# Performance work log

Hardware: AMD Instinct MI355X
Metric: run time of the kernel (lower is better)

The kernel has to match this reference:

```python
import jax, jax.numpy as jnp
import numpy as np

B, N, D, K = 8, 2048, 512, 16  # batch, points, feature dim, similar_num
EPS = 1e-8


def setup_inputs() -> dict:
    key = jax.random.key(0)
    ks = jax.random.split(key, 9)
    p = jax.random.normal(ks[0], (B, N, 3), dtype=jnp.float32)
    q = jax.random.normal(ks[1], (B, N, 3), dtype=jnp.float32)
    ffp = jax.random.normal(ks[2], (B, N, D), dtype=jnp.float32)
    ffq = jax.random.normal(ks[3], (B, N, D), dtype=jnp.float32)
    eye = jnp.eye(3, dtype=jnp.float32)
    # near-identity perturbed rotations so inverse is well-conditioned
    R1 = eye + 0.1 * jax.random.normal(ks[4], (B, N, 3, 3), dtype=jnp.float32)
    R2 = eye + 0.1 * jax.random.normal(ks[5], (B, N, 3, 3), dtype=jnp.float32)
    centroids = jax.random.randint(ks[6], (B, N), 0, 2 * N)  # FPS indices into 2N pts
    W = 0.02 * jax.random.normal(ks[7], (3, 3 * D), dtype=jnp.float32)  # refine_net pointwise linear
    b = jnp.zeros((3,), dtype=jnp.float32)
    return {"p": p, "q": q, "ffp": ffp, "ffq": ffq, "R1": R1, "R2": R2,
            "centroids": centroids, "W": W, "b": b}


def _forward(p, q, ffp, ffq, R1, R2, centroids, W, b):
    # cosine similarity between query features (ffq) and source features (ffp): [B,N,N]
    fq = ffq / (jnp.linalg.norm(ffq, axis=-1, keepdims=True) + EPS)
    fp = ffp / (jnp.linalg.norm(ffp, axis=-1, keepdims=True) + EPS)
    w1 = jnp.einsum('bqd,bpd->bqp', fq, fp)
    _, idx = jax.lax.top_k(w1, K)                      # [B,N,K] neighbor indices into ffp
    feat = jax.vmap(lambda z, i: z[i])(ffp, idx)       # batched gather -> [B,N,K,D]
    # adaptive_{avg,max}_pool2d over the K axis, then cat(avg, max): [B,N,2D]
    f_agg = jnp.concatenate([feat.mean(axis=2), feat.max(axis=2)], axis=-1)
    f1 = jnp.concatenate([ffq, f_agg], axis=-1)        # [B,N,3D]
    vec = jnp.einsum('bnd,od->bno', f1, W) + b         # refine_net -> [B,N,3]
    vec = jnp.linalg.inv(R1) @ vec[..., None]          # rotate back (R1^-1)
    vec = (jnp.linalg.inv(R2) @ vec)[..., 0]           # rotate back (R2^-1) -> [B,N,3]
    mask = (centroids >= p.shape[1]).astype(vec.dtype)[..., None]
    q_refine = q + vec * mask
    return q_refine, idx


def reference(p, q, ffp, ffq, R1, R2, centroids, W, b):
    q_refine, similar_idx = _forward(p, q, ffp, ffq, R1, R2, centroids, W, b)
    # original returns (q_cat, q_refine, q_refine, similar_idx)
    return (q, q_refine, q_refine, similar_idx)
```

## Files before the change

kernel.cpp:

```cpp
#include <hip/hip_runtime.h>
#include <math.h>

#define BB 8
#define NN 2048
#define DD 512
#define KK 16
#define BN (BB*NN)

#define QT 64
#define JSPLIT 4
#define JRANGE (NN/JSPLIT)
#define MM (16*JSPLIT)
#define SIMP 68

#define KSPLIT 384

#define OUT1 (BN*3)
#define OUT2 (2*BN*3)
#define OUT3 (3*BN*3)

typedef __attribute__((ext_vector_type(8))) short bf16x8;
typedef __attribute__((ext_vector_type(4))) float f32x4;

__device__ inline unsigned short cvt_bf16(float f) {
    unsigned int u = __float_as_uint(f);
    return (unsigned short)((u + 0x7fffu + ((u >> 16) & 1u)) >> 16);
}

__device__ inline void gload_lds16(const unsigned short* g, unsigned short* lds) {
    __builtin_amdgcn_global_load_lds((const __attribute__((address_space(1))) void*)g,
                                     (__attribute__((address_space(3))) void*)lds,
                                     16, 0, 0);
}

__global__ __launch_bounds__(256) void k_norm_np(const float* __restrict__ ffq,
                                                 const float* __restrict__ ffp,
                                                 float* __restrict__ normq,
                                                 float* __restrict__ normp,
                                                 float* __restrict__ rnp32) {
    const int row = blockIdx.x * 32 + (threadIdx.x >> 3);
    const int j   = threadIdx.x & 7;
    const bool isQ = row < BN;
    const int r = isQ ? row : row - BN;
    const float* x = (isQ ? ffq : ffp) + (size_t)r * DD;

    float B[4];
#pragma unroll
    for (int t = 0; t < 4; ++t) {
        const float* xb = x + t * 128;
        float e = xb[j];
        float rj = __fmul_rn(e, e);
#pragma unroll
        for (int i = 1; i < 16; ++i) {
            float v = xb[8 * i + j];
            rj = __fadd_rn(rj, __fmul_rn(v, v));
        }
        float s = __fadd_rn(rj, __shfl_xor(rj, 1, 8));
        float u = __fadd_rn(s,  __shfl_xor(s,  2, 8));
        float w = __fadd_rn(u,  __shfl_xor(u,  4, 8));
        B[t] = w;
    }
    if (j == 0) {
        float norm2 = __fadd_rn(__fadd_rn(B[0], B[1]), __fadd_rn(B[2], B[3]));
        float nrm = __fsqrt_rn(norm2);
        if (isQ) { normq[r] = nrm; }
        else {
            normp[r] = nrm;
            rnp32[r] = 1.0f / __fadd_rn(nrm, 1e-8f);
        }
    }
}

__global__ __launch_bounds__(256) void k_normalize(const float* __restrict__ ffq,
                                                   const float* __restrict__ ffp,
                                                   const float* __restrict__ normq,
                                                   const float* __restrict__ normp,
                                                   float* __restrict__ fqn,
                                                   float* __restrict__ fpn,
                                                   unsigned short* __restrict__ fqb,
                                                   unsigned short* __restrict__ fpb) {
    const size_t e4 = ((size_t)blockIdx.x * 256 + threadIdx.x) * 4;
    if (e4 >= (size_t)BN * DD) return;
    const int row = (int)(e4 >> 9);
    {
        float4 v = *(const float4*)(ffq + e4);
        float den = __fadd_rn(normq[row], 1e-8f);
        float4 o;
        o.x = __fdiv_rn(v.x, den); o.y = __fdiv_rn(v.y, den);
        o.z = __fdiv_rn(v.z, den); o.w = __fdiv_rn(v.w, den);
        *(float4*)(fqn + e4) = o;
        ushort4 b; b.x = cvt_bf16(o.x); b.y = cvt_bf16(o.y);
        b.z = cvt_bf16(o.z); b.w = cvt_bf16(o.w);
        *(ushort4*)(fqb + e4) = b;
    }
    {
        float4 v = *(const float4*)(ffp + e4);
        float den = __fadd_rn(normp[row], 1e-8f);
        float4 o;
        o.x = __fdiv_rn(v.x, den); o.y = __fdiv_rn(v.y, den);
        o.z = __fdiv_rn(v.z, den); o.w = __fdiv_rn(v.w, den);
        *(float4*)(fpn + e4) = o;
        ushort4 b; b.x = cvt_bf16(o.x); b.y = cvt_bf16(o.y);
        b.z = cvt_bf16(o.z); b.w = cvt_bf16(o.w);
        *(ushort4*)(fpb + e4) = b;
    }
}

#define CK 128
__global__ __launch_bounds__(256, 4) void k_phase1_m(const unsigned short* __restrict__ fqb,
                                                     const unsigned short* __restrict__ fpb,
                                                     unsigned short* __restrict__ cand) {
    __shared__ __align__(16) float simb[QT * SIMP];
    __shared__ __align__(16) unsigned short Bst[64 * CK];

    const int b  = blockIdx.x & 7;
    const int i0 = ((blockIdx.x >> 3) & 31) * QT;
    const int js = blockIdx.x >> 8;
    const int tid = threadIdx.x;
    const int w = tid >> 6, lane = tid & 63;
    const int n16 = lane & 15, quad = lane >> 4;

    const unsigned short* Aq = fqb + ((size_t)b * NN + i0 + w * 16 + n16) * DD + quad * 8;

    unsigned long long ktop[16];
#pragma unroll
    for (int r = 0; r < 16; ++r) ktop[r] = 0ull;

    const int qq = tid >> 2;
    const int st = tid & 3;
    const size_t bNN = (size_t)b * NN;

    for (int jt = 0; jt < JRANGE / 64; ++jt) {
        const int j0g = js * JRANGE + jt * 64;

        f32x4 acc[4];
#pragma unroll
        for (int ct = 0; ct < 4; ++ct) acc[ct] = (f32x4){0.f, 0.f, 0.f, 0.f};

        for (int kc = 0; kc < 4; ++kc) {
            __syncthreads();
#pragma unroll
            for (int l = 0; l < 4; ++l) {
                const int r  = (w * 4 + l) * 4 + quad;
                const int sb = n16 ^ (r & 15);
                const unsigned short* gsrc =
                    fpb + (bNN + j0g + r) * DD + kc * CK + sb * 8;
                gload_lds16(gsrc, &Bst[(w * 4 + l) * 512]);
            }
            int koff = kc * 128;
            asm volatile("" : "+v"(koff));
            bf16x8 a0 = *(const bf16x8*)(Aq + koff);
            bf16x8 a1 = *(const bf16x8*)(Aq + koff + 32);
            bf16x8 a2 = *(const bf16x8*)(Aq + koff + 64);
            bf16x8 a3 = *(const bf16x8*)(Aq + koff + 96);
            __syncthreads();
#pragma unroll
            for (int k4 = 0; k4 < 4; ++k4) {
                const bf16x8 af = (k4 == 0) ? a0 : (k4 == 1) ? a1 : (k4 == 2) ? a2 : a3;
#pragma unroll
                for (int ct = 0; ct < 4; ++ct) {
                    const int r  = ct * 16 + n16;
                    const int cb = (k4 * 4 + quad) ^ (r & 15);
                    bf16x8 bfr = *(const bf16x8*)&Bst[r * CK + cb * 8];
                    acc[ct] = __builtin_amdgcn_mfma_f32_16x16x32_bf16(
                        af, bfr, acc[ct], 0, 0, 0);
                }
            }
        }

        __syncthreads();
#pragma unroll
        for (int ct = 0; ct < 4; ++ct)
#pragma unroll
            for (int r = 0; r < 4; ++r)
                simb[(w * 16 + quad * 4 + r) * SIMP + ct * 16 + n16] = acc[ct][r];
        __syncthreads();

        unsigned long long nk[16];
#pragma unroll
        for (int t4 = 0; t4 < 4; ++t4) {
            const float4 v4 = *(const float4*)&simb[qq * SIMP + st * 16 + t4 * 4];
            const float vv[4] = {v4.x, v4.y, v4.z, v4.w};
#pragma unroll
            for (int u = 0; u < 4; ++u) {
                const float cvf = __fadd_rn(vv[u], 0.0f);
                const unsigned int ub  = __float_as_uint(cvf);
                const unsigned int ord = ub ^ (((unsigned int)((int)ub >> 31)) | 0x80000000u);
                const unsigned int jg  = (unsigned int)(j0g + st * 16 + t4 * 4 + u);
                nk[t4 * 4 + u] = ((unsigned long long)ord << 32)
                               | (unsigned long long)(~jg);
            }
        }
#pragma unroll
        for (int k = 2; k <= 16; k <<= 1) {
#pragma unroll
            for (int j = k >> 1; j > 0; j >>= 1) {
#pragma unroll
                for (int i = 0; i < 16; ++i) {
                    const int l = i ^ j;
                    if (l > i) {
                        const bool up = ((i & k) == 0);
                        const unsigned long long a = nk[i], bq = nk[l];
                        const bool sw = up ? (a > bq) : (a < bq);
                        nk[i] = sw ? bq : a;
                        nk[l] = sw ? a : bq;
                    }
                }
            }
        }
        unsigned long long mg[16];
#pragma unroll
        for (int i = 0; i < 16; ++i) {
            const unsigned long long a = ktop[i], bq = nk[15 - i];
            mg[i] = (a > bq) ? a : bq;
        }
#pragma unroll
        for (int j = 8; j > 0; j >>= 1) {
#pragma unroll
            for (int i = 0; i < 16; ++i) {
                const int l = i ^ j;
                if (l > i) {
                    const unsigned long long a = mg[i], bq = mg[l];
                    const bool sw = a > bq;
                    mg[i] = sw ? bq : a;
                    mg[l] = sw ? a : bq;
                }
            }
        }
#pragma unroll
        for (int i = 0; i < 16; ++i) ktop[i] = mg[i];
    }

    __syncthreads();
    int p = 15;
    const size_t base = ((size_t)b * NN + i0 + qq) * MM + (size_t)js * 16;
    for (int m = 0; m < 16; ++m) {
        const unsigned long long myk = (p >= 0) ? ktop[p] : 0ull;
        unsigned long long wk = myk;
        unsigned long long ok;
        ok = __shfl_xor(wk, 1, 4); if (ok > wk) wk = ok;
        ok = __shfl_xor(wk, 2, 4); if (ok > wk) wk = ok;
        if (p >= 0 && myk == wk) --p;
        if (st == 0) cand[base + m] = (unsigned short)(~(unsigned int)wk);
    }
}

#define JTILE 64
#define BK 16
#define LDP 68
__global__ __launch_bounds__(256, 4) void k_phase1_v(const float* __restrict__ ffq,
                                                     const float* __restrict__ ffp,
                                                     const float* __restrict__ rnp32,
                                                     unsigned short* __restrict__ cand) {
    __shared__ __align__(16) float As[BK * LDP];
    __shared__ __align__(16) float Bs[BK * LDP];
    __shared__ __align__(16) float simb[QT * SIMP];

    const int b  = blockIdx.x & 7;
    const int i0 = ((blockIdx.x >> 3) & 31) * QT;
    const int js = blockIdx.x >> 8;
    const int tid = threadIdx.x;
    const int tx = tid & 15, ty = tid >> 4;

    const float* Abase = ffq + ((size_t)b * NN + i0) * DD;
    const float* Bbase = ffp + (size_t)b * NN * DD;

    float tv[16]; int tix[16];
#pragma unroll
    for (int r = 0; r < 16; ++r) { tv[r] = -INFINITY; tix[r] = -1; }

    const int lrow = tid >> 2;
    const int lseg = (tid & 3) * 4;
    const int qq = tid >> 2;
    const int st = tid & 3;

    for (int jt = 0; jt < JRANGE / JTILE; ++jt) {
        const int j0 = js * JRANGE + jt * JTILE;
        float acc[4][4];
#pragma unroll
        for (int r = 0; r < 4; ++r)
#pragma unroll
            for (int c = 0; c < 4; ++c) acc[r][c] = 0.0f;

        for (int kt = 0; kt < DD / BK; ++kt) {
            const int k0 = kt * BK;
            __syncthreads();
            float4 av = *(const float4*)(Abase + (size_t)lrow * DD + k0 + lseg);
            float4 bv = *(const float4*)(Bbase + (size_t)(j0 + lrow) * DD + k0 + lseg);
            As[(lseg + 0) * LDP + lrow] = av.x; As[(lseg + 1) * LDP + lrow] = av.y;
            As[(lseg + 2) * LDP + lrow] = av.z; As[(lseg + 3) * LDP + lrow] = av.w;
            Bs[(lseg + 0) * LDP + lrow] = bv.x; Bs[(lseg + 1) * LDP + lrow] = bv.y;
            Bs[(lseg + 2) * LDP + lrow] = bv.z; Bs[(lseg + 3) * LDP + lrow] = bv.w;
            __syncthreads();
#pragma unroll
            for (int kk = 0; kk < BK; ++kk) {
                const float4 a4 = *(const float4*)&As[kk * LDP + ty * 4];
                const float4 b4 = *(const float4*)&Bs[kk * LDP + tx * 4];
                const float ar[4] = {a4.x, a4.y, a4.z, a4.w};
                const float br[4] = {b4.x, b4.y, b4.z, b4.w};
#pragma unroll
                for (int r = 0; r < 4; ++r)
#pragma unroll
                    for (int c = 0; c < 4; ++c)
                        acc[r][c] = fmaf(ar[r], br[c], acc[r][c]);
            }
        }
        float rp[4];
#pragma unroll
        for (int c = 0; c < 4; ++c) rp[c] = rnp32[b * NN + j0 + tx * 4 + c];
#pragma unroll
        for (int r = 0; r < 4; ++r) {
            float4 v4;
            v4.x = acc[r][0] * rp[0]; v4.y = acc[r][1] * rp[1];
            v4.z = acc[r][2] * rp[2]; v4.w = acc[r][3] * rp[3];
            *(float4*)&simb[(ty * 4 + r) * SIMP + tx * 4] = v4;
        }
        __syncthreads();

#pragma unroll
        for (int t = 0; t < 16; ++t) {
            const int jl = st * 16 + t;
            const float v = simb[qq * SIMP + jl];
            const int jg = j0 + jl;
            if (v > tv[0]) {
#pragma unroll
                for (int r = 0; r < 15; ++r) {
                    const bool up = tv[r + 1] < v;
                    const float nv = up ? tv[r + 1] : ((tv[r] < v) ? v : tv[r]);
                    const int   ni = up ? tix[r + 1] : ((tv[r] < v) ? jg : tix[r]);
                    tv[r] = nv; tix[r] = ni;
                }
                if (tv[15] < v) { tv[15] = v; tix[15] = jg; }
            }
        }
        __syncthreads();
    }

    int p = 15;
    const size_t base = ((size_t)b * NN + i0 + qq) * MM + (size_t)js * 16;
    for (int m = 0; m < 16; ++m) {
        float cv = (p >= 0) ? tv[p] : -INFINITY;
        int   ci = (p >= 0) ? tix[p] : -1;
        float ov; int oi;
        ov = __shfl_xor(cv, 1, 4); oi = __shfl_xor(ci, 1, 4);
        if (ov > cv || (ov == cv && (unsigned)oi < (unsigned)ci)) { cv = ov; ci = oi; }
        ov = __shfl_xor(cv, 2, 4); oi = __shfl_xor(ci, 2, 4);
        if (ov > cv || (ov == cv && (unsigned)oi < (unsigned)ci)) { cv = ov; ci = oi; }
        if (p >= 0 && tv[p] == cv && tix[p] == ci) --p;
        if (st == 0) cand[base + m] = (unsigned short)ci;
    }
}

__device__ inline void inv3_apply(const double* a, double x0, double x1, double x2,
                                  double& y0, double& y1, double& y2) {
    double c00 = a[4]*a[8] - a[5]*a[7];
    double c01 = a[2]*a[7] - a[1]*a[8];
    double c02 = a[1]*a[5] - a[2]*a[4];
    double c10 = a[5]*a[6] - a[3]*a[8];
    double c11 = a[0]*a[8] - a[2]*a[6];
    double c12 = a[2]*a[3] - a[0]*a[5];
    double c20 = a[3]*a[7] - a[4]*a[6];
    double c21 = a[1]*a[6] - a[0]*a[7];
    double c22 = a[0]*a[4] - a[1]*a[3];
    double det = a[0]*c00 + a[1]*c10 + a[2]*c20;
    double id = 1.0 / det;
    y0 = (c00*x0 + c01*x1 + c02*x2) * id;
    y1 = (c10*x0 + c11*x1 + c12*x2) * id;
    y2 = (c20*x0 + c21*x1 + c22*x2) * id;
}

#define STG_S 67
template <bool PRE>
__device__ inline void phase2_body(
        const float* __restrict__ qin, const float* __restrict__ ffq,
        const float* __restrict__ ffp, const float* __restrict__ R1,
        const float* __restrict__ R2, const int* __restrict__ cent,
        const float* __restrict__ W, const float* __restrict__ bvec,
        const float* __restrict__ normq, const float* __restrict__ normp,
        const float* __restrict__ fqn, const float* __restrict__ fpn,
        const unsigned short* __restrict__ cand, float* __restrict__ out) {
    static_assert(KSPLIT == 384, "chunk split at c=6 assumes KSPLIT==384");
    static_assert(MM * STG_S >= 2 * DD, "meanf/maxf overlay needs 2*DD floats");
    const int b = blockIdx.x & 7;
    const int i = blockIdx.x >> 3;
    const int tid = threadIdx.x;
    const size_t qi = (size_t)b * NN + i;

    __shared__ float sfqn[DD];
    __shared__ int cj[MM];
    __shared__ float pden_s[MM];
    __shared__ float sv[MM];
    __shared__ int sel[KK];
    __shared__ __align__(16) float stg[MM * STG_S];
    __shared__ float red[3][4];
    float* const meanf = stg;
    float* const maxf  = stg + DD;

    if (PRE) {
        for (int d = tid; d < DD; d += 256)
            sfqn[d] = fqn[qi * DD + d];
    } else {
        const float qden = __fadd_rn(normq[qi], 1e-8f);
        for (int d = tid; d < DD; d += 256)
            sfqn[d] = __fdiv_rn(ffq[qi * DD + d], qden);
    }
    if (tid < MM) {
        int j = (int)cand[qi * MM + tid];
        cj[tid] = j;
        if (!PRE) pden_s[tid] = __fadd_rn(normp[(size_t)b * NN + j], 1e-8f);
    }
    __syncthreads();

    const int srow = tid >> 2;
    const int slan = tid & 3;
    const float* fprow = (PRE ? fpn : ffp) + ((size_t)b * NN + cj[srow]) * DD;
    const float pd = (!PRE) ? pden_s[tid < MM ? tid : 0] : 1.0f;
    float acc1 = 0.0f, acc2 = 0.0f;

    auto stg_write = [&](const float4* P) {
#pragma unroll
        for (int i4 = 0; i4 < 4; ++i4) {
            const int off = srow * STG_S + i4 * 16 + slan * 4;
            stg[off + 0] = P[i4].x; stg[off + 1] = P[i4].y;
            stg[off + 2] = P[i4].z; stg[off + 3] = P[i4].w;
        }
    };
    auto ld_chunk = [&](float4* P, int c) {
#pragma unroll
        for (int i4 = 0; i4 < 4; ++i4)
            P[i4] = *(const float4*)(fprow + c * 64 + i4 * 16 + slan * 4);
    };
    auto chain = [&](int c, float& acc) {
        const int d0 = c * 64;
        const float* s = stg + tid * STG_S;
        if (PRE) {
#pragma unroll
            for (int k = 0; k < 64; ++k)
                acc = fmaf(sfqn[d0 + k], s[k], acc);
        } else {
#pragma unroll
            for (int k = 0; k < 64; ++k)
                acc = fmaf(sfqn[d0 + k], __fdiv_rn(s[k], pd), acc);
        }
    };

    float4 pA[4], pB[4];
    ld_chunk(pA, 0);
#pragma unroll
    for (int ch = 0; ch < 4; ++ch) {
        {
            const int c0 = 2 * ch;
            stg_write(pA);
            ld_chunk(pB, c0 + 1);
            __syncthreads();
            if (tid < MM) chain(c0, (c0 < 6) ? acc1 : acc2);
            __syncthreads();
        }
        {
            const int c1 = 2 * ch + 1;
            stg_write(pB);
            if (ch < 3) ld_chunk(pA, c1 + 1);
            __syncthreads();
            if (tid < MM) chain(c1, (c1 < 6) ? acc1 : acc2);
            __syncthreads();
        }
    }
    if (tid < MM) sv[tid] = __fadd_rn(acc1, acc2);
    __syncthreads();

    if (tid < MM) {
        const float v = sv[tid]; const int jj = cj[tid];
        int rank = 0;
        for (int t = 0; t < MM; ++t) {
            const float vt = sv[t]; const int jo = cj[t];
            rank += (vt > v) || (vt == v && jo < jj);
        }
        if (rank < KK) {
            sel[rank] = jj;
            out[(size_t)OUT3 + qi * KK + rank] = (float)jj;
        }
    }
    __syncthreads();

    for (int d = tid; d < DD; d += 256) {
        float sum = 0.0f, mx = -INFINITY;
#pragma unroll
        for (int k = 0; k < KK; ++k) {
            float v = ffp[((size_t)b * NN + sel[k]) * DD + d];
            sum += v; mx = fmaxf(mx, v);
        }
        meanf[d] = sum * (1.0f / 16.0f);
        maxf[d]  = mx;
    }
    __syncthreads();

    float a0 = 0.f, a1 = 0.f, a2 = 0.f;
    for (int d = tid; d < DD; d += 256) {
        const float x = ffq[qi * DD + d], m = meanf[d], mx = maxf[d];
        a0 = fmaf(W[d],        x, a0); a0 = fmaf(W[512 + d],        m, a0); a0 = fmaf(W[1024 + d],        mx, a0);
        a1 = fmaf(W[1536 + d], x, a1); a1 = fmaf(W[1536 + 512 + d], m, a1); a1 = fmaf(W[1536 + 1024 + d], mx, a1);
        a2 = fmaf(W[3072 + d], x, a2); a2 = fmaf(W[3072 + 512 + d], m, a2); a2 = fmaf(W[3072 + 1024 + d], mx, a2);
    }
#pragma unroll
    for (int off = 32; off > 0; off >>= 1) {
        a0 += __shfl_down(a0, off, 64);
        a1 += __shfl_down(a1, off, 64);
        a2 += __shfl_down(a2, off, 64);
    }
    const int lane = tid & 63, wid = tid >> 6;
    if (lane == 0) { red[0][wid] = a0; red[1][wid] = a1; red[2][wid] = a2; }
    __syncthreads();

    if (tid == 0) {
        double v0 = (double)bvec[0] + red[0][0] + red[0][1] + red[0][2] + red[0][3];
        double v1 = (double)bvec[1] + red[1][0] + red[1][1] + red[1][2] + red[1][3];
        double v2 = (double)bvec[2] + red[2][0] + red[2][1] + red[2][2] + red[2][3];
        double r1[9], r2[9];
#pragma unroll
        for (int t = 0; t < 9; ++t) { r1[t] = R1[qi * 9 + t]; r2[t] = R2[qi * 9 + t]; }
        double u0, u1, u2, w0, w1, w2;
        inv3_apply(r1, v0, v1, v2, u0, u1, u2);
        inv3_apply(r2, u0, u1, u2, w0, w1, w2);
        const float mask = (cent[qi] >= NN) ? 1.0f : 0.0f;
        const float q0 = qin[qi * 3 + 0], q1 = qin[qi * 3 + 1], q2 = qin[qi * 3 + 2];
        out[qi * 3 + 0] = q0; out[qi * 3 + 1] = q1; out[qi * 3 + 2] = q2;
        const float o0 = q0 + (float)w0 * mask;
        const float o1 = q1 + (float)w1 * mask;
        const float o2 = q2 + (float)w2 * mask;
        out[OUT1 + qi * 3 + 0] = o0; out[OUT1 + qi * 3 + 1] = o1; out[OUT1 + qi * 3 + 2] = o2;
        out[OUT2 + qi * 3 + 0] = o0; out[OUT2 + qi * 3 + 1] = o1; out[OUT2 + qi * 3 + 2] = o2;
    }
}

__global__ __launch_bounds__(256, 8) void k_phase2_f(
        const float* qin, const float* ffq, const float* ffp, const float* R1,
        const float* R2, const int* cent, const float* W, const float* bvec,
        const float* fqn, const float* fpn, const unsigned short* cand, float* out) {
    phase2_body<true>(qin, ffq, ffp, R1, R2, cent, W, bvec,
                      nullptr, nullptr, fqn, fpn, cand, out);
}

__global__ __launch_bounds__(256, 8) void k_phase2_v(
        const float* qin, const float* ffq, const float* ffp, const float* R1,
        const float* R2, const int* cent, const float* W, const float* bvec,
        const float* normq, const float* normp, const unsigned short* cand, float* out) {
    phase2_body<false>(qin, ffq, ffp, R1, R2, cent, W, bvec,
                       normq, normp, nullptr, nullptr, cand, out);
}

extern "C" void kernel_launch(void* const* d_in, const int* in_sizes, int n_in,
                              void* d_out, int out_size, void* d_ws, size_t ws_size,
                              hipStream_t stream) {
    (void)in_sizes; (void)n_in; (void)out_size;
    const float* q   = (const float*)d_in[1];
    const float* ffp = (const float*)d_in[2];
    const float* ffq = (const float*)d_in[3];
    const float* R1  = (const float*)d_in[4];
    const float* R2  = (const float*)d_in[5];
    const int*   ct  = (const int*)d_in[6];
    const float* W   = (const float*)d_in[7];
    const float* bb  = (const float*)d_in[8];
    float* out = (float*)d_out;

    float* normq = (float*)d_ws;
    float* normp = normq + BN;
    float* rnp32 = normp + BN;
    unsigned short* cand = (unsigned short*)(rnp32 + BN);
    float* fqn = (float*)(cand + (size_t)BN * MM);
    float* fpn = fqn + (size_t)BN * DD;
    unsigned short* fqb = (unsigned short*)(fpn + (size_t)BN * DD);
    unsigned short* fpb = fqb + (size_t)BN * DD;

    const size_t need = (size_t)BN * (35 * 4 + 2 * DD * 4 + 2 * DD * 2);

    k_norm_np<<<dim3((2 * BN) / 32), dim3(256), 0, stream>>>(ffq, ffp, normq, normp, rnp32);

    if (ws_size >= need) {
        k_normalize<<<dim3((BN * DD) / 1024), dim3(256), 0, stream>>>(
            ffq, ffp, normq, normp, fqn, fpn, fqb, fpb);
        k_phase1_m<<<dim3(BB * (NN / QT) * JSPLIT), dim3(256), 0, stream>>>(fqb, fpb, cand);
        k_phase2_f<<<dim3(BB * NN), dim3(256), 0, stream>>>(q, ffq, ffp, R1, R2, ct, W, bb,
                                                            fqn, fpn, cand, out);
    } else {
        k_phase1_v<<<dim3(BB * (NN / QT) * JSPLIT), dim3(256), 0, stream>>>(ffq, ffp, rnp32, cand);
        k_phase2_v<<<dim3(BB * NN), dim3(256), 0, stream>>>(q, ffq, ffp, R1, R2, ct, W, bb,
                                                            normq, normp, cand, out);
    }
}
```

Baseline: 426.4 us.

## Run phase-2 rescoring with one wavefront per query and register-held candidate rows

Phase-2 blocks drop from 256 threads to a single 64-thread wavefront, where each lane owns one candidate. Each lane loads its own candidate feature row straight into registers (double-buffered float4 chunks) and computes the dot product there, replacing the shared-memory staging and its block barriers. Removing the cross-wave reduction also removes one shared array and one barrier. The trade-offs are much higher register pressure from 32 float4 buffers and uncoalesced per-lane row loads, with fewer threads left for the gather and projection loops.

```diff
diff --git a/kernel.cpp b/kernel.cpp
--- a/kernel.cpp
+++ b/kernel.cpp
@@ -369,7 +369,6 @@
     y2 = (c20*x0 + c21*x1 + c22*x2) * id;
 }
 
-#define STG_S 67
 template <bool PRE>
 __device__ inline void phase2_body(
         const float* __restrict__ qin, const float* __restrict__ ffq,
@@ -380,109 +379,90 @@
         const float* __restrict__ fqn, const float* __restrict__ fpn,
         const unsigned short* __restrict__ cand, float* __restrict__ out) {
     static_assert(KSPLIT == 384, "chunk split at c=6 assumes KSPLIT==384");
-    static_assert(MM * STG_S >= 2 * DD, "meanf/maxf overlay needs 2*DD floats");
     const int b = blockIdx.x & 7;
     const int i = blockIdx.x >> 3;
-    const int tid = threadIdx.x;
+    const int t = threadIdx.x;
     const size_t qi = (size_t)b * NN + i;
 
-    __shared__ float sfqn[DD];
-    __shared__ int cj[MM];
-    __shared__ float pden_s[MM];
+    __shared__ __align__(16) float sbuf[2 * DD];
     __shared__ float sv[MM];
+    __shared__ int cjs[MM];
     __shared__ int sel[KK];
-    __shared__ __align__(16) float stg[MM * STG_S];
-    __shared__ float red[3][4];
-    float* const meanf = stg;
-    float* const maxf  = stg + DD;
+    float* const sfqn  = sbuf;
+    float* const meanf = sbuf;
+    float* const maxf  = sbuf + DD;
 
     if (PRE) {
-        for (int d = tid; d < DD; d += 256)
+        for (int d = t; d < DD; d += 64)
             sfqn[d] = fqn[qi * DD + d];
     } else {
         const float qden = __fadd_rn(normq[qi], 1e-8f);
-        for (int d = tid; d < DD; d += 256)
+        for (int d = t; d < DD; d += 64)
             sfqn[d] = __fdiv_rn(ffq[qi * DD + d], qden);
     }
-    if (tid < MM) {
-        int j = (int)cand[qi * MM + tid];
-        cj[tid] = j;
-        if (!PRE) pden_s[tid] = __fadd_rn(normp[(size_t)b * NN + j], 1e-8f);
-    }
+    const int j = (int)cand[qi * MM + t];
+    cjs[t] = j;
+    const float pd = PRE ? 1.0f : __fadd_rn(normp[(size_t)b * NN + j], 1e-8f);
+    const float* fprow = (PRE ? fpn : ffp) + ((size_t)b * NN + j) * DD;
     __syncthreads();
 
-    const int srow = tid >> 2;
-    const int slan = tid & 3;
-    const float* fprow = (PRE ? fpn : ffp) + ((size_t)b * NN + cj[srow]) * DD;
-    const float pd = (!PRE) ? pden_s[tid < MM ? tid : 0] : 1.0f;
     float acc1 = 0.0f, acc2 = 0.0f;
-
-    auto stg_write = [&](const float4* P) {
-#pragma unroll
-        for (int i4 = 0; i4 < 4; ++i4) {
-            const int off = srow * STG_S + i4 * 16 + slan * 4;
-            stg[off + 0] = P[i4].x; stg[off + 1] = P[i4].y;
-            stg[off + 2] = P[i4].z; stg[off + 3] = P[i4].w;
-        }
+    float4 bufA[16], bufB[16];
+
+    auto ldc = [&](float4* P, int c) {
+#pragma unroll
+        for (int m = 0; m < 16; ++m)
+            P[m] = *(const float4*)(fprow + c * 64 + m * 4);
     };
-    auto ld_chunk = [&](float4* P, int c) {
-#pragma unroll
-        for (int i4 = 0; i4 < 4; ++i4)
-            P[i4] = *(const float4*)(fprow + c * 64 + i4 * 16 + slan * 4);
+    auto chn = [&](const float4* P, int c, float& acc) {
+        const int d0 = c * 64;
+        if (PRE) {
+#pragma unroll
+            for (int m = 0; m < 16; ++m) {
+                acc = fmaf(sfqn[d0 + m * 4 + 0], P[m].x, acc);
+                acc = fmaf(sfqn[d0 + m * 4 + 1], P[m].y, acc);
+                acc = fmaf(sfqn[d0 + m * 4 + 2], P[m].z, acc);
+                acc = fmaf(sfqn[d0 + m * 4 + 3], P[m].w, acc);
+            }
+        } else {
+#pragma unroll
+            for (int m = 0; m < 16; ++m) {
+                acc = fmaf(sfqn[d0 + m * 4 + 0], __fdiv_rn(P[m].x, pd), acc);
+                acc = fmaf(sfqn[d0 + m * 4 + 1], __fdiv_rn(P[m].y, pd), acc);
+                acc = fmaf(sfqn[d0 + m * 4 + 2], __fdiv_rn(P[m].z, pd), acc);
+                acc = fmaf(sfqn[d0 + m * 4 + 3], __fdiv_rn(P[m].w, pd), acc);
+            }
+        }
     };
-    auto chain = [&](int c, float& acc) {
-        const int d0 = c * 64;
-        const float* s = stg + tid * STG_S;
-        if (PRE) {
-#pragma unroll
-            for (int k = 0; k < 64; ++k)
-                acc = fmaf(sfqn[d0 + k], s[k], acc);
-        } else {
-#pragma unroll
-            for (int k = 0; k < 64; ++k)
-                acc = fmaf(sfqn[d0 + k], __fdiv_rn(s[k], pd), acc);
-        }
-    };
-
-    float4 pA[4], pB[4];
-    ld_chunk(pA, 0);
-#pragma unroll
-    for (int ch = 0; ch < 4; ++ch) {
-        {
-            const int c0 = 2 * ch;
-            stg_write(pA);
-            ld_chunk(pB, c0 + 1);
-            __syncthreads();
-            if (tid < MM) chain(c0, (c0 < 6) ? acc1 : acc2);
-            __syncthreads();
-        }
-        {
-            const int c1 = 2 * ch + 1;
-            stg_write(pB);
-            if (ch < 3) ld_chunk(pA, c1 + 1);
-            __syncthreads();
-            if (tid < MM) chain(c1, (c1 < 6) ? acc1 : acc2);
-            __syncthreads();
-        }
-    }
-    if (tid < MM) sv[tid] = __fadd_rn(acc1, acc2);
+
+    ldc(bufA, 0);
+#pragma unroll
+    for (int h = 0; h < 4; ++h) {
+        const int c0 = 2 * h;
+        ldc(bufB, c0 + 1);
+        chn(bufA, c0, (c0 < 6) ? acc1 : acc2);
+        const int c1 = 2 * h + 1;
+        if (h < 3) ldc(bufA, c1 + 1);
+        chn(bufB, c1, (c1 < 6) ? acc1 : acc2);
+    }
+    sv[t] = __fadd_rn(acc1, acc2);
     __syncthreads();
 
-    if (tid < MM) {
-        const float v = sv[tid]; const int jj = cj[tid];
+    {
+        const float v = sv[t];
         int rank = 0;
-        for (int t = 0; t < MM; ++t) {
-            const float vt = sv[t]; const int jo = cj[t];
-            rank += (vt > v) || (vt == v && jo < jj);
+        for (int tt = 0; tt < MM; ++tt) {
+            const float vt = sv[tt]; const int jo = cjs[tt];
+            rank += (vt > v) || (vt == v && jo < j);
         }
         if (rank < KK) {
-            sel[rank] = jj;
-            out[(size_t)OUT3 + qi * KK + rank] = (float)jj;
+            sel[rank] = j;
+            out[(size_t)OUT3 + qi * KK + rank] = (float)j;
         }
     }
     __syncthreads();
 
-    for (int d = tid; d < DD; d += 256) {
+    for (int d = t; d < DD; d += 64) {
         float sum = 0.0f, mx = -INFINITY;
 #pragma unroll
         for (int k = 0; k < KK; ++k) {
@@ -495,7 +475,7 @@
     __syncthreads();
 
     float a0 = 0.f, a1 = 0.f, a2 = 0.f;
-    for (int d = tid; d < DD; d += 256) {
+    for (int d = t; d < DD; d += 64) {
         const float x = ffq[qi * DD + d], m = meanf[d], mx = maxf[d];
         a0 = fmaf(W[d],        x, a0); a0 = fmaf(W[512 + d],        m, a0); a0 = fmaf(W[1024 + d],        mx, a0);
         a1 = fmaf(W[1536 + d], x, a1); a1 = fmaf(W[1536 + 512 + d], m, a1); a1 = fmaf(W[1536 + 1024 + d], mx, a1);
@@ -507,17 +487,14 @@
         a1 += __shfl_down(a1, off, 64);
         a2 += __shfl_down(a2, off, 64);
     }
-    const int lane = tid & 63, wid = tid >> 6;
-    if (lane == 0) { red[0][wid] = a0; red[1][wid] = a1; red[2][wid] = a2; }
-    __syncthreads();
-
-    if (tid == 0) {
-        double v0 = (double)bvec[0] + red[0][0] + red[0][1] + red[0][2] + red[0][3];
-        double v1 = (double)bvec[1] + red[1][0] + red[1][1] + red[1][2] + red[1][3];
-        double v2 = (double)bvec[2] + red[2][0] + red[2][1] + red[2][2] + red[2][3];
+
+    if (t == 0) {
+        double v0 = (double)bvec[0] + a0;
+        double v1 = (double)bvec[1] + a1;
+        double v2 = (double)bvec[2] + a2;
         double r1[9], r2[9];
 #pragma unroll
-        for (int t = 0; t < 9; ++t) { r1[t] = R1[qi * 9 + t]; r2[t] = R2[qi * 9 + t]; }
+        for (int u = 0; u < 9; ++u) { r1[u] = R1[qi * 9 + u]; r2[u] = R2[qi * 9 + u]; }
         double u0, u1, u2, w0, w1, w2;
         inv3_apply(r1, v0, v1, v2, u0, u1, u2);
         inv3_apply(r2, u0, u1, u2, w0, w1, w2);
@@ -532,7 +509,7 @@
     }
 }
 
-__global__ __launch_bounds__(256, 8) void k_phase2_f(
+__global__ __launch_bounds__(64) void k_phase2_f(
         const float* qin, const float* ffq, const float* ffp, const float* R1,
         const float* R2, const int* cent, const float* W, const float* bvec,
         const float* fqn, const float* fpn, const unsigned short* cand, float* out) {
@@ -540,7 +517,7 @@
                       nullptr, nullptr, fqn, fpn, cand, out);
 }
 
-__global__ __launch_bounds__(256, 8) void k_phase2_v(
+__global__ __launch_bounds__(64) void k_phase2_v(
         const float* qin, const float* ffq, const float* ffp, const float* R1,
         const float* R2, const int* cent, const float* W, const float* bvec,
         const float* normq, const float* normp, const unsigned short* cand, float* out) {
@@ -579,11 +556,11 @@
         k_normalize<<<dim3((BN * DD) / 1024), dim3(256), 0, stream>>>(
             ffq, ffp, normq, normp, fqn, fpn, fqb, fpb);
         k_phase1_m<<<dim3(BB * (NN / QT) * JSPLIT), dim3(256), 0, stream>>>(fqb, fpb, cand);
-        k_phase2_f<<<dim3(BB * NN), dim3(256), 0, stream>>>(q, ffq, ffp, R1, R2, ct, W, bb,
-                                                            fqn, fpn, cand, out);
+        k_phase2_f<<<dim3(BB * NN), dim3(64), 0, stream>>>(q, ffq, ffp, R1, R2, ct, W, bb,
+                                                           fqn, fpn, cand, out);
     } else {
         k_phase1_v<<<dim3(BB * (NN / QT) * JSPLIT), dim3(256), 0, stream>>>(ffq, ffp, rnp32, cand);
-        k_phase2_v<<<dim3(BB * NN), dim3(256), 0, stream>>>(q, ffq, ffp, R1, R2, ct, W, bb,
-                                                            normq, normp, cand, out);
-    }
-}
+        k_phase2_v<<<dim3(BB * NN), dim3(64), 0, stream>>>(q, ffq, ffp, R1, R2, ct, W, bb,
+                                                           normq, normp, cand, out);
+    }
+}
```

Result: slower. 671.6 us (+57.5%).
